# Kernel optimization log

Measured on AMD Instinct MI355X. Metric: run time of the kernel, lower is better.

Reference implementation:

```python
import jax, jax.numpy as jnp
import numpy as np

EPS = 1e-8  # matches torch F.cosine_similarity default eps


def setup_inputs() -> dict:
    key = jax.random.key(0)
    k1, k2, k3 = jax.random.split(key, 3)
    B, S, Q, T, D = 1, 5, 512, 64, 2048
    supp = jax.random.normal(k1, (B, S, T, D), dtype=jnp.float32)
    query = jax.random.normal(k2, (B, Q, T, D), dtype=jnp.float32)
    query_ys = jax.random.randint(k3, (Q,), 0, S, dtype=jnp.int64)
    return {"supp": supp, "query": query, "query_ys": query_ys}


def reference(supp, query, query_ys):
    # supp: [B, S, T, D], query: [B, Q, T, D]
    # Pool once over T (mathematically identical to repeat-then-mean).
    sp = supp.mean(axis=-2)   # [B, S, D]
    qp = query.mean(axis=-2)  # [B, Q, D]
    # Pairwise cosine similarity over D -> [B, Q, S]
    num = jnp.einsum('bqd,bsd->bqs', qp, sp)
    qn = jnp.linalg.norm(qp, axis=-1)  # [B, Q]
    sn = jnp.linalg.norm(sp, axis=-1)  # [B, S]
    denom = jnp.maximum(qn[:, :, None] * sn[:, None, :], EPS)
    dist = (num / denom)[0]  # squeeze(0) -> [Q, S]
    # Cross-entropy over the num_supp (class) axis
    logp = jax.nn.log_softmax(dist, axis=-1)
    loss = -jnp.take_along_axis(logp, query_ys[:, None], axis=1).mean()
    return (loss, 1.0 - dist)
```

## Files before the change

kernel.cpp:

```cpp
#include <hip/hip_runtime.h>
#include <hip/hip_bf16.h>

#define S_DIM 5
#define Q_DIM 512
#define T_DIM 64
#define D_DIM 2048
#define EPS_CS 1e-8f


__device__ __forceinline__ float wave_reduce_sum(float v) {
    #pragma unroll
    for (int off = 32; off > 0; off >>= 1)
        v += __shfl_down(v, off, 64);
    return v;
}

__global__ __launch_bounds__(512) void supp_pool_kernel(
    const float* __restrict__ supp, float* __restrict__ sp, float* __restrict__ sn)
{
    const int s   = blockIdx.x;
    const int tid = threadIdx.x;
    const float4* base = (const float4*)(supp + (size_t)s * T_DIM * D_DIM);

    float4 acc = make_float4(0.f, 0.f, 0.f, 0.f);
    #pragma unroll 8
    for (int t = 0; t < T_DIM; ++t) {
        float4 v = base[t * (D_DIM / 4) + tid];
        acc.x += v.x; acc.y += v.y; acc.z += v.z; acc.w += v.w;
    }
    const float inv = 1.0f / (float)T_DIM;
    acc.x *= inv; acc.y *= inv; acc.z *= inv; acc.w *= inv;

    ((float4*)(sp + (size_t)s * D_DIM))[tid] = acc;

    float sq = acc.x * acc.x + acc.y * acc.y + acc.z * acc.z + acc.w * acc.w;
    float r = wave_reduce_sum(sq);

    __shared__ float lds[8];
    const int wave = tid >> 6, lane = tid & 63;
    if (lane == 0) lds[wave] = r;
    __syncthreads();
    if (tid == 0) {
        float tot = 0.f;
        #pragma unroll
        for (int w = 0; w < 8; ++w) tot += lds[w];
        sn[s] = sqrtf(tot);
    }
}

__global__ __launch_bounds__(512) void query_pool_dot_kernel(
    const float* __restrict__ query, const float* __restrict__ sp,
    float* __restrict__ num, float* __restrict__ sq)
{
    const int q   = blockIdx.x;
    const int tid = threadIdx.x;
    const float4* base = (const float4*)(query + (size_t)q * T_DIM * D_DIM);

    float4 acc = make_float4(0.f, 0.f, 0.f, 0.f);
    #pragma unroll 8
    for (int t = 0; t < T_DIM; ++t) {
        float4 v = base[t * (D_DIM / 4) + tid];
        acc.x += v.x; acc.y += v.y; acc.z += v.z; acc.w += v.w;
    }
    const float inv = 1.0f / (float)T_DIM;
    acc.x *= inv; acc.y *= inv; acc.z *= inv; acc.w *= inv;

    float vals[6];
    vals[5] = acc.x * acc.x + acc.y * acc.y + acc.z * acc.z + acc.w * acc.w;
    #pragma unroll
    for (int s = 0; s < S_DIM; ++s) {
        float4 sv = ((const float4*)(sp + (size_t)s * D_DIM))[tid];
        vals[s] = acc.x * sv.x + acc.y * sv.y + acc.z * sv.z + acc.w * sv.w;
    }

    __shared__ float lds[8][6];
    const int wave = tid >> 6, lane = tid & 63;
    #pragma unroll
    for (int k = 0; k < 6; ++k) {
        float r = wave_reduce_sum(vals[k]);
        if (lane == 0) lds[wave][k] = r;
    }
    __syncthreads();
    if (tid < 6) {
        float r = 0.f;
        #pragma unroll
        for (int w = 0; w < 8; ++w) r += lds[w][tid];
        if (tid < S_DIM) num[(size_t)q * S_DIM + tid] = r;
        else             sq[q] = r;
    }
}

__global__ __launch_bounds__(512) void finalize_kernel(
    const float* __restrict__ num, const float* __restrict__ sq,
    const float* __restrict__ sn, const int* __restrict__ ys,
    float* __restrict__ out)
{
    const int q = threadIdx.x;

    const float qn = sqrtf(sq[q]);
    float dist[S_DIM];
    #pragma unroll
    for (int s = 0; s < S_DIM; ++s) {
        float d = num[(size_t)q * S_DIM + s] / fmaxf(qn * sn[s], EPS_CS);
        dist[s] = d;
        out[1 + (size_t)q * S_DIM + s] = 1.0f - d;
    }

    float m = dist[0];
    #pragma unroll
    for (int s = 1; s < S_DIM; ++s) m = fmaxf(m, dist[s]);
    float sum = 0.f;
    #pragma unroll
    for (int s = 0; s < S_DIM; ++s) sum += expf(dist[s] - m);
    const float lse = m + logf(sum);

    int y = ys[q];
    if (y < 0) y = 0; if (y >= S_DIM) y = S_DIM - 1;
    const float nll = lse - dist[y];

    float r = wave_reduce_sum(nll);
    __shared__ float lds[8];
    const int wave = q >> 6, lane = q & 63;
    if (lane == 0) lds[wave] = r;
    __syncthreads();
    if (q == 0) {
        float tot = 0.f;
        #pragma unroll
        for (int w = 0; w < 8; ++w) tot += lds[w];
        out[0] = tot * (1.0f / (float)Q_DIM);
    }
}

extern "C" void kernel_launch(void* const* d_in, const int* in_sizes, int n_in,
                              void* d_out, int out_size, void* d_ws, size_t ws_size,
                              hipStream_t stream) {
    const float* supp  = (const float*)d_in[0];
    const float* query = (const float*)d_in[1];
    const int*   ys    = (const int*)d_in[2];
    float* out = (float*)d_out;

    float* ws  = (float*)d_ws;
    float* sp  = ws;
    float* sn  = ws + 10240;
    float* num = ws + 10248;
    float* sq  = ws + 12808;

    supp_pool_kernel<<<S_DIM, 512, 0, stream>>>(supp, sp, sn);
    query_pool_dot_kernel<<<Q_DIM, 512, 0, stream>>>(query, sp, num, sq);
    finalize_kernel<<<1, 512, 0, stream>>>(num, sq, sn, ys, out);
}
```

Measured before the change: 60.32 us.

## Pool supp and query in one launch, move dot products and softmax into separate kernel

The supp pooling and query pooling now run together in a single kernel with S+Q blocks, so the 5-block supp launch no longer serialises ahead of the heavy query pass. Pooled query vectors are written to workspace, and a new dot kernel (one wave per query) computes the cosine distances and per-query NLL. A small final kernel reduces the loss. Loads use nontemporal hints with deeper unrolling. The cost is an extra round trip through workspace for the pooled query vectors (4 MB write plus read) and the same number of launches as before.

```diff
diff --git a/kernel.cpp b/kernel.cpp
--- a/kernel.cpp
+++ b/kernel.cpp
@@ -7,6 +7,12 @@
 #define D_DIM 2048
 #define EPS_CS 1e-8f
 
+typedef float f32x4 __attribute__((ext_vector_type(4)));
+
+#define WS_SP    0
+#define WS_QP    10240
+#define WS_NORMS 1058816
+#define WS_NLL   1059336
 
 __device__ __forceinline__ float wave_reduce_sum(float v) {
     #pragma unroll
@@ -15,23 +21,32 @@
     return v;
 }
 
-__global__ __launch_bounds__(512) void supp_pool_kernel(
-    const float* __restrict__ supp, float* __restrict__ sp, float* __restrict__ sn)
+__global__ __launch_bounds__(512) void pool_kernel(
+    const float* __restrict__ supp, const float* __restrict__ query,
+    float* __restrict__ sp, float* __restrict__ qp, float* __restrict__ norms)
 {
-    const int s   = blockIdx.x;
+    const int b   = blockIdx.x;
     const int tid = threadIdx.x;
-    const float4* base = (const float4*)(supp + (size_t)s * T_DIM * D_DIM);
 
-    float4 acc = make_float4(0.f, 0.f, 0.f, 0.f);
-    #pragma unroll 8
+    const float* src = (b < S_DIM)
+        ? supp  + (size_t)b * T_DIM * D_DIM
+        : query + (size_t)(b - S_DIM) * T_DIM * D_DIM;
+    float* dst = (b < S_DIM)
+        ? sp + (size_t)b * D_DIM
+        : qp + (size_t)(b - S_DIM) * D_DIM;
+
+    const f32x4* base = (const f32x4*)src;
+
+    f32x4 acc = {0.f, 0.f, 0.f, 0.f};
+    #pragma unroll 16
     for (int t = 0; t < T_DIM; ++t) {
-        float4 v = base[t * (D_DIM / 4) + tid];
-        acc.x += v.x; acc.y += v.y; acc.z += v.z; acc.w += v.w;
+        f32x4 v = __builtin_nontemporal_load(&base[t * (D_DIM / 4) + tid]);
+        acc += v;
     }
     const float inv = 1.0f / (float)T_DIM;
-    acc.x *= inv; acc.y *= inv; acc.z *= inv; acc.w *= inv;
+    acc *= inv;
 
-    ((float4*)(sp + (size_t)s * D_DIM))[tid] = acc;
+    ((f32x4*)dst)[tid] = acc;
 
     float sq = acc.x * acc.x + acc.y * acc.y + acc.z * acc.z + acc.w * acc.w;
     float r = wave_reduce_sum(sq);
@@ -44,81 +59,69 @@
         float tot = 0.f;
         #pragma unroll
         for (int w = 0; w < 8; ++w) tot += lds[w];
-        sn[s] = sqrtf(tot);
+        norms[b] = sqrtf(tot);
     }
 }
 
-__global__ __launch_bounds__(512) void query_pool_dot_kernel(
-    const float* __restrict__ query, const float* __restrict__ sp,
-    float* __restrict__ num, float* __restrict__ sq)
+__global__ __launch_bounds__(512) void dot_kernel(
+    const float* __restrict__ sp, const float* __restrict__ qp,
+    const float* __restrict__ norms, const int* __restrict__ ys,
+    float* __restrict__ out, float* __restrict__ nll)
 {
-    const int q   = blockIdx.x;
-    const int tid = threadIdx.x;
-    const float4* base = (const float4*)(query + (size_t)q * T_DIM * D_DIM);
+    const int wave = threadIdx.x >> 6;
+    const int lane = threadIdx.x & 63;
+    const int q    = blockIdx.x * 8 + wave;
 
-    float4 acc = make_float4(0.f, 0.f, 0.f, 0.f);
-    #pragma unroll 8
-    for (int t = 0; t < T_DIM; ++t) {
-        float4 v = base[t * (D_DIM / 4) + tid];
-        acc.x += v.x; acc.y += v.y; acc.z += v.z; acc.w += v.w;
-    }
-    const float inv = 1.0f / (float)T_DIM;
-    acc.x *= inv; acc.y *= inv; acc.z *= inv; acc.w *= inv;
+    const f32x4* qv4 = (const f32x4*)(qp + (size_t)q * D_DIM);
 
-    float vals[6];
-    vals[5] = acc.x * acc.x + acc.y * acc.y + acc.z * acc.z + acc.w * acc.w;
+    float dots[S_DIM];
     #pragma unroll
-    for (int s = 0; s < S_DIM; ++s) {
-        float4 sv = ((const float4*)(sp + (size_t)s * D_DIM))[tid];
-        vals[s] = acc.x * sv.x + acc.y * sv.y + acc.z * sv.z + acc.w * sv.w;
+    for (int s = 0; s < S_DIM; ++s) dots[s] = 0.f;
+
+    #pragma unroll
+    for (int i = 0; i < D_DIM / 4 / 64; ++i) {
+        const int idx = lane + i * 64;
+        f32x4 v = qv4[idx];
+        #pragma unroll
+        for (int s = 0; s < S_DIM; ++s) {
+            f32x4 sv = ((const f32x4*)(sp + (size_t)s * D_DIM))[idx];
+            dots[s] += v.x * sv.x + v.y * sv.y + v.z * sv.z + v.w * sv.w;
+        }
     }
 
-    __shared__ float lds[8][6];
-    const int wave = tid >> 6, lane = tid & 63;
     #pragma unroll
-    for (int k = 0; k < 6; ++k) {
-        float r = wave_reduce_sum(vals[k]);
-        if (lane == 0) lds[wave][k] = r;
-    }
-    __syncthreads();
-    if (tid < 6) {
-        float r = 0.f;
+    for (int s = 0; s < S_DIM; ++s)
+        dots[s] = wave_reduce_sum(dots[s]);
+
+    if (lane == 0) {
+        const float qn = norms[S_DIM + q];
+        float dist[S_DIM];
         #pragma unroll
-        for (int w = 0; w < 8; ++w) r += lds[w][tid];
-        if (tid < S_DIM) num[(size_t)q * S_DIM + tid] = r;
-        else             sq[q] = r;
+        for (int s = 0; s < S_DIM; ++s) {
+            float d = dots[s] / fmaxf(qn * norms[s], EPS_CS);
+            dist[s] = d;
+            out[1 + (size_t)q * S_DIM + s] = 1.0f - d;
+        }
+        float m = dist[0];
+        #pragma unroll
+        for (int s = 1; s < S_DIM; ++s) m = fmaxf(m, dist[s]);
+        float sum = 0.f;
+        #pragma unroll
+        for (int s = 0; s < S_DIM; ++s) sum += expf(dist[s] - m);
+        const float lse = m + logf(sum);
+
+        int y = ys[q];
+        if (y < 0) y = 0;
+        if (y >= S_DIM) y = S_DIM - 1;
+        nll[q] = lse - dist[y];
     }
 }
 
-__global__ __launch_bounds__(512) void finalize_kernel(
-    const float* __restrict__ num, const float* __restrict__ sq,
-    const float* __restrict__ sn, const int* __restrict__ ys,
-    float* __restrict__ out)
+__global__ __launch_bounds__(512) void loss_kernel(
+    const float* __restrict__ nll, float* __restrict__ out)
 {
     const int q = threadIdx.x;
-
-    const float qn = sqrtf(sq[q]);
-    float dist[S_DIM];
-    #pragma unroll
-    for (int s = 0; s < S_DIM; ++s) {
-        float d = num[(size_t)q * S_DIM + s] / fmaxf(qn * sn[s], EPS_CS);
-        dist[s] = d;
-        out[1 + (size_t)q * S_DIM + s] = 1.0f - d;
-    }
-
-    float m = dist[0];
-    #pragma unroll
-    for (int s = 1; s < S_DIM; ++s) m = fmaxf(m, dist[s]);
-    float sum = 0.f;
-    #pragma unroll
-    for (int s = 0; s < S_DIM; ++s) sum += expf(dist[s] - m);
-    const float lse = m + logf(sum);
-
-    int y = ys[q];
-    if (y < 0) y = 0; if (y >= S_DIM) y = S_DIM - 1;
-    const float nll = lse - dist[y];
-
-    float r = wave_reduce_sum(nll);
+    float r = wave_reduce_sum(nll[q]);
     __shared__ float lds[8];
     const int wave = q >> 6, lane = q & 63;
     if (lane == 0) lds[wave] = r;
@@ -139,13 +142,13 @@
     const int*   ys    = (const int*)d_in[2];
     float* out = (float*)d_out;
 
-    float* ws  = (float*)d_ws;
-    float* sp  = ws;
-    float* sn  = ws + 10240;
-    float* num = ws + 10248;
-    float* sq  = ws + 12808;
+    float* ws    = (float*)d_ws;
+    float* sp    = ws + WS_SP;
+    float* qp    = ws + WS_QP;
+    float* norms = ws + WS_NORMS;
+    float* nll   = ws + WS_NLL;
 
-    supp_pool_kernel<<<S_DIM, 512, 0, stream>>>(supp, sp, sn);
-    query_pool_dot_kernel<<<Q_DIM, 512, 0, stream>>>(query, sp, num, sq);
-    finalize_kernel<<<1, 512, 0, stream>>>(num, sq, sn, ys, out);
+    pool_kernel<<<S_DIM + Q_DIM, 512, 0, stream>>>(supp, query, sp, qp, norms);
+    dot_kernel<<<Q_DIM / 8, 512, 0, stream>>>(sp, qp, norms, ys, out, nll);
+    loss_kernel<<<1, 512, 0, stream>>>(nll, out);
 }
```

After: 65.70 us. 8.9% more time.
